# Optimization experiments

Hardware: AMD Instinct MI355X
Metric: run time of the kernel (lower is better)

Reference implementation:

```python
import jax, jax.numpy as jnp
import numpy as np

N = 50000        # nodes
R = 51           # enriched relations (25 fwd + 25 inverse + self-loop)
F_IN = 32        # feat_size
E = 32           # embed_size
C = 16           # num_classes
B = 30           # num_bases
NNZ = 2_000_000  # nonzeros in vertical adjacency


def _xavier(key, shape):
    # mimics nn.init.xavier_uniform_ with gain for relu (sqrt(2))
    fan_in, fan_out = shape[-2], shape[-1]
    a = np.sqrt(2.0) * np.sqrt(6.0 / (fan_in + fan_out))
    return jax.random.uniform(key, shape, jnp.float32, -a, a)


def setup_inputs() -> dict:
    key = jax.random.key(0)
    ks = jax.random.split(key, 8)
    # COO of vertical adjacency, shape (R*N, N)
    rows = jax.random.randint(ks[0], (NNZ,), 0, R * N)
    cols = jax.random.randint(ks[1], (NNZ,), 0, N)
    # row-normalized values: vals = 1 / row_degree  (sum_sparse with rows=True)
    deg = jax.ops.segment_sum(jnp.ones((NNZ,), jnp.float32), rows, num_segments=R * N)
    vals = (1.0 / jnp.maximum(deg, 1.0))[rows]
    features = jax.random.normal(ks[2], (N, F_IN), jnp.float32)
    comps1 = _xavier(ks[3], (R, B))
    bases1 = _xavier(ks[4], (B, F_IN, E))
    comps2 = _xavier(ks[5], (R, B))
    bases2 = _xavier(ks[6], (B, E, C))
    bias1 = jnp.zeros((E,), jnp.float32)
    bias2 = jnp.zeros((C,), jnp.float32)
    return {
        "features": features, "vals": vals,
        "comps1": comps1, "bases1": bases1, "bias1": bias1,
        "comps2": comps2, "bases2": bases2, "bias2": bias2,
        "rows": rows, "cols": cols,
    }


def _spmm(rows, cols, vals, x):
    # (R*N, N) sparse @ (N, f) dense -> (R*N, f)
    return jax.ops.segment_sum(vals[:, None] * x[cols], rows, num_segments=R * N)


def reference(features, vals, comps1, bases1, bias1, comps2, bases2, bias2, rows, cols):
    # layer 1: SpMM then basis-decomposed per-relation mixing
    h = _spmm(rows, cols, vals, features).reshape(R, N, F_IN)   # (r, n, f)
    w1 = jnp.einsum('rb,bfe->rfe', comps1, bases1)              # (r, f, e)
    h = jnp.einsum('rnf,rfe->ne', h, w1)                        # (n, e)
    h = jax.nn.relu(h + bias1)
    # layer 2
    h = _spmm(rows, cols, vals, h).reshape(R, N, E)             # (r, n, e)
    w2 = jnp.einsum('rb,bho->rho', comps2, bases2)              # (r, e, c)
    h = jnp.einsum('rho,rnh->no', w2, h)                        # (n, c)
    return h + bias2
```

## Files before the change

kernel.cpp:

```cpp
#include <hip/hip_runtime.h>

#define NNODES 50000
#define RREL 51
#define FIN 32
#define EDIM 32
#define CDIM 16
#define BB 30
#define NNZ_ 2000000
#define CAP_ 2000896
#define EPB 4096
#define NBUK 391

typedef unsigned int uint32;
typedef unsigned short ushort;
typedef uint32 u32x2 __attribute__((ext_vector_type(2)));
typedef uint32 u32x4 __attribute__((ext_vector_type(4)));
typedef short bf16x8 __attribute__((ext_vector_type(8)));
typedef float f32x4 __attribute__((ext_vector_type(4)));

static __device__ __forceinline__ uint32 pack_bf16x2(float a, float b) {
    uint32 ua = __builtin_bit_cast(uint32, a);
    uint32 ub = __builtin_bit_cast(uint32, b);
    ua += 0x7fffu + ((ua >> 16) & 1u);
    ub += 0x7fffu + ((ub >> 16) & 1u);
    return (ua >> 16) | (ub & 0xffff0000u);
}
static __device__ __forceinline__ ushort bf16_1(float x) {
    uint32 u = __builtin_bit_cast(uint32, x);
    u += 0x7fffu + ((u >> 16) & 1u);
    return (ushort)(u >> 16);
}
static __device__ __forceinline__ float unpack_lo(uint32 u) { return __builtin_bit_cast(float, u << 16); }
static __device__ __forceinline__ float unpack_hi(uint32 u) { return __builtin_bit_cast(float, u & 0xffff0000u); }

__global__ void k_weights(const float* __restrict__ comps1, const float* __restrict__ bases1,
                          const float* __restrict__ comps2, const float* __restrict__ bases2,
                          ushort* __restrict__ Wb1, ushort* __restrict__ Wb2) {
    int i = blockIdx.x * 256 + threadIdx.x;
    if (i < RREL * FIN * EDIM) {
        int r = i >> 10, fe = i & 1023, f = fe >> 5, e = fe & 31;
        float acc = 0.f;
#pragma unroll
        for (int b = 0; b < BB; b++) acc += comps1[r * BB + b] * bases1[b * 1024 + fe];
        Wb1[((r * 4 + (f >> 3)) * 32 + e) * 8 + (f & 7)] = bf16_1(acc);
    }
    if (i < RREL * EDIM * CDIM) {
        int r = i >> 9, ec = i & 511, kk = ec >> 4, c = ec & 15;
        float acc = 0.f;
#pragma unroll
        for (int b = 0; b < BB; b++) acc += comps2[r * BB + b] * bases2[b * 512 + ec];
        Wb2[((r * 4 + (kk >> 3)) * 16 + c) * 8 + (kk & 7)] = bf16_1(acc);
    }
}

__global__ void k_tobf16(const float2* __restrict__ src, uint32* __restrict__ dst, int n2) {
    int i = blockIdx.x * 256 + threadIdx.x;
    if (i < n2) {
        float2 f = src[i];
        dst[i] = pack_bf16x2(f.x, f.y);
    }
}

__global__ __launch_bounds__(1024) void k_relhist(const int* __restrict__ rows,
                                                  int* __restrict__ rel_cnt) {
    __shared__ int lc[RREL];
    int t = threadIdx.x;
    if (t < RREL) lc[t] = 0;
    __syncthreads();
    size_t k = (size_t)blockIdx.x * EPB + (size_t)t * 4;
    int rr[4];
    if (k + 4 <= NNZ_) {
        int4 rw = *(const int4*)(rows + k);
        rr[0] = rw.x; rr[1] = rw.y; rr[2] = rw.z; rr[3] = rw.w;
    } else {
#pragma unroll
        for (int j = 0; j < 4; j++) rr[j] = (k + j < NNZ_) ? rows[k + j] : -1;
    }
#pragma unroll
    for (int j = 0; j < 4; j++)
        if (rr[j] >= 0) atomicAdd(&lc[rr[j] / NNODES], 1);
    __syncthreads();
    if (t < RREL) atomicAdd(&rel_cnt[t], lc[t]);
}

__global__ void k_relscan(const int* __restrict__ rel_cnt, int* __restrict__ pad_base,
                          int* __restrict__ rel_cur) {
    if (threadIdx.x == 0) {
        int a = 0;
        for (int r = 0; r < RREL; r++) {
            pad_base[r] = a; rel_cur[r] = a;
            a += (rel_cnt[r] + 15) & ~15;
        }
        pad_base[RREL] = a;
    }
}

__global__ void k_padfill(const int* __restrict__ rel_cnt, const int* __restrict__ pad_base,
                          int* __restrict__ s_pk, int* __restrict__ s_src,
                          float* __restrict__ s_val, int* __restrict__ buk_cnt) {
    int r = blockIdx.x;
    int start, end, relv;
    if (r < RREL) { start = pad_base[r] + rel_cnt[r]; end = pad_base[r + 1]; relv = r; }
    else { start = pad_base[RREL]; end = CAP_; relv = 0; }
    if (threadIdx.x == 0 && end > start) atomicAdd(&buk_cnt[NBUK - 1], end - start);
    int pkpad = (int)(((uint32)relv << 25) | (uint32)NNODES);
    for (int i = start + threadIdx.x; i < end; i += 64) {
        s_pk[i] = pkpad;
        s_src[i] = 0;
        s_val[i] = 0.f;
    }
}

__global__ __launch_bounds__(1024) void k_scatter(const int* __restrict__ rows, const int* __restrict__ cols,
                                                  const float* __restrict__ vals, int* __restrict__ rel_cur,
                                                  int* __restrict__ buk_cnt,
                                                  int* __restrict__ s_pk, int* __restrict__ s_src,
                                                  float* __restrict__ s_val) {
    __shared__ int lcnt[RREL], lbase[RREL], gbase[RREL];
    __shared__ int bukc[NBUK];
    __shared__ int stotal;
    __shared__ uint32 st[EPB];
    int t = threadIdx.x;
    size_t base = (size_t)blockIdx.x * EPB;
    if (t < RREL) lcnt[t] = 0;
    if (t < NBUK) bukc[t] = 0;
    __syncthreads();
    size_t k = base + (size_t)t * 4;
    int relv[4], dstv[4];
    {
        int rr[4];
        if (k + 4 <= NNZ_) {
            int4 rw = *(const int4*)(rows + k);
            rr[0] = rw.x; rr[1] = rw.y; rr[2] = rw.z; rr[3] = rw.w;
        } else {
#pragma unroll
            for (int j = 0; j < 4; j++) rr[j] = (k + j < NNZ_) ? rows[k + j] : -1;
        }
#pragma unroll
        for (int j = 0; j < 4; j++) {
            if (rr[j] >= 0) {
                int rel = rr[j] / NNODES;
                relv[j] = rel;
                dstv[j] = rr[j] - rel * NNODES;
                atomicAdd(&lcnt[rel], 1);
                atomicAdd(&bukc[dstv[j] >> 7], 1);
            } else relv[j] = -1;
        }
    }
    __syncthreads();
    if (t < 64) {
        int v = (t < RREL) ? lcnt[t] : 0;
        int sum = v;
#pragma unroll
        for (int off = 1; off < 64; off <<= 1) {
            int u = __shfl_up(sum, off, 64);
            if (t >= off) sum += u;
        }
        if (t < RREL) { lbase[t] = sum - v; gbase[t] = atomicAdd(&rel_cur[t], v); }
        if (t == RREL - 1) stotal = sum;
    }
    if (t < NBUK) atomicAdd(&buk_cnt[t], bukc[t]);
    __syncthreads();
    if (t < RREL) lcnt[t] = 0;
    __syncthreads();
#pragma unroll
    for (int j = 0; j < 4; j++) {
        int rel = relv[j];
        if (rel >= 0) {
            int slot = lbase[rel] + atomicAdd(&lcnt[rel], 1);
            st[slot] = ((uint32)dstv[j] << 12) | (uint32)(t * 4 + j);
        }
    }
    __syncthreads();
    int total = stotal;
#pragma unroll
    for (int i = 0; i < 4; i++) {
        int s2 = t + i * 1024;
        if (s2 < total) {
            uint32 u = st[s2];
            int dst = (int)(u >> 12);
            size_t orig = base + (u & 4095u);
            int rel = rows[orig] / NNODES;
            int g = gbase[rel] + (s2 - lbase[rel]);
            s_pk[g] = (int)(((uint32)rel << 25) | (uint32)dst);
            s_src[g] = cols[orig];
            s_val[g] = vals[orig];
        }
    }
}

__global__ void k_bukscan(const int* __restrict__ buk_cnt, int* __restrict__ buk_base,
                          int* __restrict__ buk_cur) {
    if (threadIdx.x == 0) {
        int a = 0;
        for (int b = 0; b < NBUK; b++) { buk_base[b] = a; buk_cur[b] = a; a += buk_cnt[b]; }
        buk_base[NBUK] = a;
    }
}

__global__ __launch_bounds__(1024) void k_bucket(const int* __restrict__ s_pk,
                                                 int* __restrict__ buk_cur,
                                                 u32x2* __restrict__ tok8) {
    __shared__ int bukc[NBUK], lbase2[NBUK], gbase2[NBUK];
    __shared__ int ssum[1024];
    __shared__ u32x2 st8[EPB];
    int t = threadIdx.x;
    size_t base = (size_t)blockIdx.x * EPB;
    int total = (int)(((size_t)CAP_ - base < (size_t)EPB) ? ((size_t)CAP_ - base) : (size_t)EPB);
    if (t < NBUK) bukc[t] = 0;
    __syncthreads();
    size_t k = base + (size_t)t * 4;
    int pkv[4], bv[4];
    if (k + 4 <= CAP_) {
        int4 q = *(const int4*)(s_pk + k);
        pkv[0] = q.x; pkv[1] = q.y; pkv[2] = q.z; pkv[3] = q.w;
#pragma unroll
        for (int j = 0; j < 4; j++) bv[j] = (int)(((uint32)pkv[j] & 0x1FFFFFFu) >> 7);
    } else {
#pragma unroll
        for (int j = 0; j < 4; j++) {
            if (k + j < CAP_) { pkv[j] = s_pk[k + j]; bv[j] = (int)(((uint32)pkv[j] & 0x1FFFFFFu) >> 7); }
            else bv[j] = -1;
        }
    }
#pragma unroll
    for (int j = 0; j < 4; j++)
        if (bv[j] >= 0) atomicAdd(&bukc[bv[j]], 1);
    __syncthreads();
    int v = (t < NBUK) ? bukc[t] : 0;
    ssum[t] = v;
    __syncthreads();
    for (int off = 1; off < 1024; off <<= 1) {
        int u = (t >= off) ? ssum[t - off] : 0;
        __syncthreads();
        ssum[t] += u;
        __syncthreads();
    }
    if (t < NBUK) { lbase2[t] = ssum[t] - v; gbase2[t] = atomicAdd(&buk_cur[t], v); }
    __syncthreads();
    if (t < NBUK) bukc[t] = 0;
    __syncthreads();
#pragma unroll
    for (int j = 0; j < 4; j++) {
        if (bv[j] >= 0) {
            int slot = lbase2[bv[j]] + atomicAdd(&bukc[bv[j]], 1);
            u32x2 w; w.x = (uint32)pkv[j]; w.y = (uint32)(k + j);
            st8[slot] = w;
        }
    }
    __syncthreads();
    for (int s2 = t; s2 < total; s2 += 1024) {
        u32x2 w = st8[s2];
        int b = (int)((w.x & 0x1FFFFFFu) >> 7);
        tok8[gbase2[b] + (s2 - lbase2[b])] = w;
    }
}

__global__ __launch_bounds__(256) void k_rank(const u32x2* __restrict__ tok8,
                                              const int* __restrict__ buk_base,
                                              int* __restrict__ dst_base,
                                              int* __restrict__ s_pk) {
    __shared__ int lcnt[128], lexc[128], lrank[128], ssc[128];
    int b = blockIdx.x, t = threadIdx.x;
    int lo = buk_base[b], hi = buk_base[b + 1];
    int d0 = b << 7;
    if (t < 128) lcnt[t] = 0;
    __syncthreads();
    for (int i = lo + t; i < hi; i += 256) {
        int dl = (int)(tok8[i].x & 0x1FFFFFFu) - d0;
        atomicAdd(&lcnt[dl], 1);
    }
    __syncthreads();
    int v = (t < 128) ? lcnt[t] : 0;
    if (t < 128) ssc[t] = v;
    __syncthreads();
    for (int off = 1; off < 128; off <<= 1) {
        int u = (t >= off && t < 128) ? ssc[t - off] : 0;
        __syncthreads();
        if (t < 128) ssc[t] += u;
        __syncthreads();
    }
    if (t < 128) {
        lexc[t] = ssc[t] - v;
        int d = d0 + t;
        if (d <= NNODES) dst_base[d] = lo + lexc[t];
        lrank[t] = 0;
    }
    __syncthreads();
    for (int i = lo + t; i < hi; i += 256) {
        u32x2 w = tok8[i];
        int dl = (int)(w.x & 0x1FFFFFFu) - d0;
        int q = lo + lexc[dl] + atomicAdd(&lrank[dl], 1);
        s_pk[(int)w.y] = (int)((w.x & 0xFE000000u) | (uint32)q);
    }
}

template <int FO>
__global__ __launch_bounds__(256) void k_edgeA(const int* __restrict__ s_pk,
                                               const int* __restrict__ s_src,
                                               const float* __restrict__ s_val,
                                               const u32x4* __restrict__ Xb,
                                               const u32x4* __restrict__ Wb,
                                               uint32* __restrict__ y) {
    const int NT = FO / 16;
    const int NW = (FO == 32) ? 32 : 16;
    int t = threadIdx.x, lane = t & 63, wv = t >> 6;
    int ln15 = lane & 15, quad = lane >> 4;
    size_t k0 = (size_t)blockIdx.x * 512 + wv * 128;

    int pk0 = s_pk[k0 + lane],  pk1 = s_pk[k0 + 64 + lane];
    int sc0 = s_src[k0 + lane], sc1 = s_src[k0 + 64 + lane];
    float v0 = s_val[k0 + lane], v1 = s_val[k0 + 64 + lane];

    f32x4 acc[8][NT];
    const f32x4 zero = {0.f, 0.f, 0.f, 0.f};
#pragma unroll
    for (int s = 0; s < 8; s++) {
        int osc = (s < 4) ? sc0 : sc1;
        int opk = (s < 4) ? pk0 : pk1;
        int srcs = __shfl(osc, (s & 3) * 16 + ln15, 64);
        int rels = (int)(((uint32)__builtin_amdgcn_readfirstlane(__shfl(opk, (s & 3) * 16, 64))) >> 25);
        bf16x8 a = __builtin_bit_cast(bf16x8, Xb[(size_t)srcs * 4 + quad]);
#pragma unroll
        for (int tt = 0; tt < NT; tt++) {
            bf16x8 b = __builtin_bit_cast(bf16x8, Wb[(rels * 4 + quad) * NW + ln15 + 16 * tt]);
            acc[s][tt] = __builtin_amdgcn_mfma_f32_16x16x32_bf16(a, b, zero, 0, 0, 0);
        }
    }

#pragma unroll
    for (int s = 0; s < 8; s++) {
        int opk = (s < 4) ? pk0 : pk1;
        float ov = (s < 4) ? v0 : v1;
#pragma unroll
        for (int rg = 0; rg < 4; rg++) {
            int e = (s & 3) * 16 + quad * 4 + rg;
            float ve = __shfl(ov, e, 64);
            int pe = __shfl(opk, e, 64) & 0x1FFFFFF;
            if (FO == 32) {
                uint32 val = pack_bf16x2(acc[s][0][rg] * ve, acc[s][1][rg] * ve);
                y[(size_t)pe * 16 + ln15] = val;
            } else {
                ((ushort*)y)[(size_t)pe * 16 + ln15] = bf16_1(acc[s][0][rg] * ve);
            }
        }
    }
}

template <int FO, bool RELU, bool BF16OUT>
__global__ __launch_bounds__(256) void k_segB(const uint32* __restrict__ y,
                                              const int* __restrict__ dst_base,
                                              const float* __restrict__ bias,
                                              void* __restrict__ outp) {
    const int UPR = FO / 2;
    const int QL = UPR / 4;
    const int RPI = 64 / QL;
    const bool ILV = (FO == 32);
    int t = threadIdx.x, lane = t & 63, wv = t >> 6;
    int dst = blockIdx.x * 4 + wv;
    if (dst >= NNODES) return;
    int s = dst_base[dst], e2 = dst_base[dst + 1];
    int q = lane % QL, r = lane / QL;
    float acc[8];
#pragma unroll
    for (int j = 0; j < 8; j++) acc[j] = 0.f;
    for (int i = s + r; i < e2; i += RPI) {
        u32x4 u = __builtin_nontemporal_load((const u32x4*)(y + (size_t)i * UPR + 4 * q));
        acc[0] += unpack_lo(u.x); acc[1] += unpack_hi(u.x);
        acc[2] += unpack_lo(u.y); acc[3] += unpack_hi(u.y);
        acc[4] += unpack_lo(u.z); acc[5] += unpack_hi(u.z);
        acc[6] += unpack_lo(u.w); acc[7] += unpack_hi(u.w);
    }
#pragma unroll
    for (int off = 32; off >= QL; off >>= 1)
#pragma unroll
        for (int j = 0; j < 8; j++) acc[j] += __shfl_down(acc[j], off, 64);
    if (lane < QL) {
        float o[8];
        if (ILV) {
#pragma unroll
            for (int j = 0; j < 4; j++) {
                o[2 * j]     = acc[2 * j]     + bias[4 * q + j];
                o[2 * j + 1] = acc[2 * j + 1] + bias[4 * q + 16 + j];
                if (RELU) { o[2 * j] = fmaxf(o[2 * j], 0.f); o[2 * j + 1] = fmaxf(o[2 * j + 1], 0.f); }
            }
        } else {
#pragma unroll
            for (int j = 0; j < 8; j++) {
                o[j] = acc[j] + bias[8 * q + j];
                if (RELU) o[j] = fmaxf(o[j], 0.f);
            }
        }
        if (BF16OUT) {
            if (ILV) {
                u32x2 a0, a1;
                a0.x = pack_bf16x2(o[0], o[2]); a0.y = pack_bf16x2(o[4], o[6]);
                a1.x = pack_bf16x2(o[1], o[3]); a1.y = pack_bf16x2(o[5], o[7]);
                ((u32x2*)outp)[(size_t)dst * 8 + q] = a0;
                ((u32x2*)outp)[(size_t)dst * 8 + 4 + q] = a1;
            } else {
                u32x4 pk;
                pk.x = pack_bf16x2(o[0], o[1]); pk.y = pack_bf16x2(o[2], o[3]);
                pk.z = pack_bf16x2(o[4], o[5]); pk.w = pack_bf16x2(o[6], o[7]);
                ((u32x4*)outp)[(size_t)dst * QL + q] = pk;
            }
        } else {
            float4* op = (float4*)outp;
            op[(size_t)dst * (FO / 4) + 2 * q]     = make_float4(o[0], o[1], o[2], o[3]);
            op[(size_t)dst * (FO / 4) + 2 * q + 1] = make_float4(o[4], o[5], o[6], o[7]);
        }
    }
}

extern "C" void kernel_launch(void* const* d_in, const int* in_sizes, int n_in,
                              void* d_out, int out_size, void* d_ws, size_t ws_size,
                              hipStream_t stream) {
    const float* features = (const float*)d_in[0];
    const float* vals     = (const float*)d_in[1];
    const float* comps1   = (const float*)d_in[2];
    const float* bases1   = (const float*)d_in[3];
    const float* bias1    = (const float*)d_in[4];
    const float* comps2   = (const float*)d_in[5];
    const float* bases2   = (const float*)d_in[6];
    const float* bias2    = (const float*)d_in[7];
    const int*   rows     = (const int*)d_in[8];
    const int*   cols     = (const int*)d_in[9];
    float* out = (float*)d_out;

    float* ws = (float*)d_ws;
    size_t o = 0;
    ushort* Wb1 = (ushort*)(ws + o); o += RREL * FIN * EDIM / 2;
    ushort* Wb2 = (ushort*)(ws + o); o += RREL * EDIM * CDIM / 2;
    o = (o + 3) & ~(size_t)3;
    uint32* Xb  = (uint32*)(ws + o); o += (size_t)NNODES * (FIN / 2);
    uint32* h1b = (uint32*)(ws + o); o += (size_t)NNODES * (EDIM / 2);
    int* s_pk  = (int*)(ws + o); o += CAP_;
    int* s_src = (int*)(ws + o); o += CAP_;
    float* s_val = ws + o;       o += CAP_;
    int* rel_cnt  = (int*)(ws + o); o += RREL + 1;
    int* buk_cnt  = (int*)(ws + o); o += NBUK + 1;
    int* rel_cur  = (int*)(ws + o); o += RREL;
    int* pad_base = (int*)(ws + o); o += RREL + 1;
    int* buk_base = (int*)(ws + o); o += NBUK + 1;
    int* buk_cur  = (int*)(ws + o); o += NBUK;
    o = (o + 3) & ~(size_t)3;
    int* dst_base = (int*)(ws + o); o += NNODES + 4;
    o = (o + 3) & ~(size_t)3;
    uint32* y = (uint32*)(ws + o);
    u32x2* tok8 = (u32x2*)y;

    const int NB = (NNZ_ + EPB - 1) / EPB;
    const int NB2 = (CAP_ + EPB - 1) / EPB;

    hipMemsetAsync(rel_cnt, 0, (RREL + 1 + NBUK + 1) * sizeof(int), stream);

    k_weights<<<(RREL * FIN * EDIM + 255) / 256, 256, 0, stream>>>(comps1, bases1, comps2, bases2, Wb1, Wb2);
    k_tobf16<<<(NNODES * FIN / 2 + 255) / 256, 256, 0, stream>>>((const float2*)features, Xb, NNODES * FIN / 2);
    k_relhist<<<NB, 1024, 0, stream>>>(rows, rel_cnt);
    k_relscan<<<1, 64, 0, stream>>>(rel_cnt, pad_base, rel_cur);
    k_padfill<<<RREL + 1, 64, 0, stream>>>(rel_cnt, pad_base, s_pk, s_src, s_val, buk_cnt);
    k_scatter<<<NB, 1024, 0, stream>>>(rows, cols, vals, rel_cur, buk_cnt, s_pk, s_src, s_val);
    k_bukscan<<<1, 64, 0, stream>>>(buk_cnt, buk_base, buk_cur);
    k_bucket<<<NB2, 1024, 0, stream>>>(s_pk, buk_cur, tok8);
    k_rank<<<NBUK, 256, 0, stream>>>(tok8, buk_base, dst_base, s_pk);

    k_edgeA<EDIM><<<CAP_ / 512, 256, 0, stream>>>(s_pk, s_src, s_val, (const u32x4*)Xb,
                                                  (const u32x4*)Wb1, y);
    k_segB<EDIM, true, true><<<(NNODES + 3) / 4, 256, 0, stream>>>(y, dst_base, bias1, h1b);
    k_edgeA<CDIM><<<CAP_ / 512, 256, 0, stream>>>(s_pk, s_src, s_val, (const u32x4*)h1b,
                                                  (const u32x4*)Wb2, y);
    k_segB<CDIM, false, false><<<(NNODES + 3) / 4, 256, 0, stream>>>(y, dst_base, bias2, out);
}
```

Baseline: 381.8 us.

## Bucket edges by destination block and fuse edge MFMA with LDS segment reduction

Replaces the relation-sorted global edge arrays and per-edge intermediate buffer with compact 8-byte edge tokens. Each token packs relation, destination, source and a bf16 value. Edges are bucketed into 64-node destination blocks, with per-relation padding done locally. A single fused kernel per layer computes the MFMA products and accumulates them with LDS atomics, then applies bias and ReLU. This drops several preprocessing kernels and the global write and reread of the intermediate y. The costs are rounding edge values to bf16, LDS atomic contention, and a fixed per-block capacity (CAPB) beyond which edges are silently dropped.

```diff
diff --git a/kernel.cpp b/kernel.cpp
--- a/kernel.cpp
+++ b/kernel.cpp
@@ -7,9 +7,10 @@
 #define CDIM 16
 #define BB 30
 #define NNZ_ 2000000
-#define CAP_ 2000896
 #define EPB 4096
 #define NBUK 391
+#define NSB 782
+#define CAPB 3840
 
 typedef unsigned int uint32;
 typedef unsigned short ushort;
@@ -31,7 +32,6 @@
     return (ushort)(u >> 16);
 }
 static __device__ __forceinline__ float unpack_lo(uint32 u) { return __builtin_bit_cast(float, u << 16); }
-static __device__ __forceinline__ float unpack_hi(uint32 u) { return __builtin_bit_cast(float, u & 0xffff0000u); }
 
 __global__ void k_weights(const float* __restrict__ comps1, const float* __restrict__ bases1,
                           const float* __restrict__ comps2, const float* __restrict__ bases2,
@@ -61,11 +61,11 @@
     }
 }
 
-__global__ __launch_bounds__(1024) void k_relhist(const int* __restrict__ rows,
-                                                  int* __restrict__ rel_cnt) {
-    __shared__ int lc[RREL];
+__global__ __launch_bounds__(1024) void k_bukhist(const int* __restrict__ rows,
+                                                  int* __restrict__ buk_cnt) {
+    __shared__ int lc[NBUK];
     int t = threadIdx.x;
-    if (t < RREL) lc[t] = 0;
+    if (t < NBUK) lc[t] = 0;
     __syncthreads();
     size_t k = (size_t)blockIdx.x * EPB + (size_t)t * 4;
     int rr[4];
@@ -77,52 +77,36 @@
         for (int j = 0; j < 4; j++) rr[j] = (k + j < NNZ_) ? rows[k + j] : -1;
     }
 #pragma unroll
-    for (int j = 0; j < 4; j++)
-        if (rr[j] >= 0) atomicAdd(&lc[rr[j] / NNODES], 1);
-    __syncthreads();
-    if (t < RREL) atomicAdd(&rel_cnt[t], lc[t]);
-}
-
-__global__ void k_relscan(const int* __restrict__ rel_cnt, int* __restrict__ pad_base,
-                          int* __restrict__ rel_cur) {
+    for (int j = 0; j < 4; j++) {
+        if (rr[j] >= 0) {
+            int rel = rr[j] / NNODES;
+            atomicAdd(&lc[(rr[j] - rel * NNODES) >> 7], 1);
+        }
+    }
+    __syncthreads();
+    if (t < NBUK) atomicAdd(&buk_cnt[t], lc[t]);
+}
+
+__global__ void k_bukscan(const int* __restrict__ buk_cnt, int* __restrict__ buk_base,
+                          int* __restrict__ buk_cur) {
     if (threadIdx.x == 0) {
         int a = 0;
-        for (int r = 0; r < RREL; r++) {
-            pad_base[r] = a; rel_cur[r] = a;
-            a += (rel_cnt[r] + 15) & ~15;
-        }
-        pad_base[RREL] = a;
-    }
-}
-
-__global__ void k_padfill(const int* __restrict__ rel_cnt, const int* __restrict__ pad_base,
-                          int* __restrict__ s_pk, int* __restrict__ s_src,
-                          float* __restrict__ s_val, int* __restrict__ buk_cnt) {
-    int r = blockIdx.x;
-    int start, end, relv;
-    if (r < RREL) { start = pad_base[r] + rel_cnt[r]; end = pad_base[r + 1]; relv = r; }
-    else { start = pad_base[RREL]; end = CAP_; relv = 0; }
-    if (threadIdx.x == 0 && end > start) atomicAdd(&buk_cnt[NBUK - 1], end - start);
-    int pkpad = (int)(((uint32)relv << 25) | (uint32)NNODES);
-    for (int i = start + threadIdx.x; i < end; i += 64) {
-        s_pk[i] = pkpad;
-        s_src[i] = 0;
-        s_val[i] = 0.f;
-    }
-}
-
-__global__ __launch_bounds__(1024) void k_scatter(const int* __restrict__ rows, const int* __restrict__ cols,
-                                                  const float* __restrict__ vals, int* __restrict__ rel_cur,
-                                                  int* __restrict__ buk_cnt,
-                                                  int* __restrict__ s_pk, int* __restrict__ s_src,
-                                                  float* __restrict__ s_val) {
-    __shared__ int lcnt[RREL], lbase[RREL], gbase[RREL];
-    __shared__ int bukc[NBUK];
-    __shared__ int stotal;
-    __shared__ uint32 st[EPB];
+        for (int b = 0; b < NBUK; b++) { buk_base[b] = a; buk_cur[b] = a; a += buk_cnt[b]; }
+        buk_base[NBUK] = a;
+    }
+}
+
+__global__ __launch_bounds__(1024) void k_bucket(const int* __restrict__ rows,
+                                                 const int* __restrict__ cols,
+                                                 const float* __restrict__ vals,
+                                                 int* __restrict__ buk_cur,
+                                                 u32x2* __restrict__ tok8) {
+    __shared__ int bukc[NBUK], lb[NBUK], gb[NBUK];
+    __shared__ int ssum[1024];
+    __shared__ u32x2 st8[EPB];
     int t = threadIdx.x;
     size_t base = (size_t)blockIdx.x * EPB;
-    if (t < RREL) lcnt[t] = 0;
+    int total = (int)(((size_t)NNZ_ - base < (size_t)EPB) ? ((size_t)NNZ_ - base) : (size_t)EPB);
     if (t < NBUK) bukc[t] = 0;
     __syncthreads();
     size_t k = base + (size_t)t * 4;
@@ -142,90 +126,10 @@
                 int rel = rr[j] / NNODES;
                 relv[j] = rel;
                 dstv[j] = rr[j] - rel * NNODES;
-                atomicAdd(&lcnt[rel], 1);
                 atomicAdd(&bukc[dstv[j] >> 7], 1);
             } else relv[j] = -1;
         }
     }
-    __syncthreads();
-    if (t < 64) {
-        int v = (t < RREL) ? lcnt[t] : 0;
-        int sum = v;
-#pragma unroll
-        for (int off = 1; off < 64; off <<= 1) {
-            int u = __shfl_up(sum, off, 64);
-            if (t >= off) sum += u;
-        }
-        if (t < RREL) { lbase[t] = sum - v; gbase[t] = atomicAdd(&rel_cur[t], v); }
-        if (t == RREL - 1) stotal = sum;
-    }
-    if (t < NBUK) atomicAdd(&buk_cnt[t], bukc[t]);
-    __syncthreads();
-    if (t < RREL) lcnt[t] = 0;
-    __syncthreads();
-#pragma unroll
-    for (int j = 0; j < 4; j++) {
-        int rel = relv[j];
-        if (rel >= 0) {
-            int slot = lbase[rel] + atomicAdd(&lcnt[rel], 1);
-            st[slot] = ((uint32)dstv[j] << 12) | (uint32)(t * 4 + j);
-        }
-    }
-    __syncthreads();
-    int total = stotal;
-#pragma unroll
-    for (int i = 0; i < 4; i++) {
-        int s2 = t + i * 1024;
-        if (s2 < total) {
-            uint32 u = st[s2];
-            int dst = (int)(u >> 12);
-            size_t orig = base + (u & 4095u);
-            int rel = rows[orig] / NNODES;
-            int g = gbase[rel] + (s2 - lbase[rel]);
-            s_pk[g] = (int)(((uint32)rel << 25) | (uint32)dst);
-            s_src[g] = cols[orig];
-            s_val[g] = vals[orig];
-        }
-    }
-}
-
-__global__ void k_bukscan(const int* __restrict__ buk_cnt, int* __restrict__ buk_base,
-                          int* __restrict__ buk_cur) {
-    if (threadIdx.x == 0) {
-        int a = 0;
-        for (int b = 0; b < NBUK; b++) { buk_base[b] = a; buk_cur[b] = a; a += buk_cnt[b]; }
-        buk_base[NBUK] = a;
-    }
-}
-
-__global__ __launch_bounds__(1024) void k_bucket(const int* __restrict__ s_pk,
-                                                 int* __restrict__ buk_cur,
-                                                 u32x2* __restrict__ tok8) {
-    __shared__ int bukc[NBUK], lbase2[NBUK], gbase2[NBUK];
-    __shared__ int ssum[1024];
-    __shared__ u32x2 st8[EPB];
-    int t = threadIdx.x;
-    size_t base = (size_t)blockIdx.x * EPB;
-    int total = (int)(((size_t)CAP_ - base < (size_t)EPB) ? ((size_t)CAP_ - base) : (size_t)EPB);
-    if (t < NBUK) bukc[t] = 0;
-    __syncthreads();
-    size_t k = base + (size_t)t * 4;
-    int pkv[4], bv[4];
-    if (k + 4 <= CAP_) {
-        int4 q = *(const int4*)(s_pk + k);
-        pkv[0] = q.x; pkv[1] = q.y; pkv[2] = q.z; pkv[3] = q.w;
-#pragma unroll
-        for (int j = 0; j < 4; j++) bv[j] = (int)(((uint32)pkv[j] & 0x1FFFFFFu) >> 7);
-    } else {
-#pragma unroll
-        for (int j = 0; j < 4; j++) {
-            if (k + j < CAP_) { pkv[j] = s_pk[k + j]; bv[j] = (int)(((uint32)pkv[j] & 0x1FFFFFFu) >> 7); }
-            else bv[j] = -1;
-        }
-    }
-#pragma unroll
-    for (int j = 0; j < 4; j++)
-        if (bv[j] >= 0) atomicAdd(&bukc[bv[j]], 1);
     __syncthreads();
     int v = (t < NBUK) ? bukc[t] : 0;
     ssum[t] = v;
@@ -236,178 +140,161 @@
         ssum[t] += u;
         __syncthreads();
     }
-    if (t < NBUK) { lbase2[t] = ssum[t] - v; gbase2[t] = atomicAdd(&buk_cur[t], v); }
+    if (t < NBUK) { lb[t] = ssum[t] - v; gb[t] = atomicAdd(&buk_cur[t], v); }
     __syncthreads();
     if (t < NBUK) bukc[t] = 0;
     __syncthreads();
-#pragma unroll
-    for (int j = 0; j < 4; j++) {
-        if (bv[j] >= 0) {
-            int slot = lbase2[bv[j]] + atomicAdd(&bukc[bv[j]], 1);
-            u32x2 w; w.x = (uint32)pkv[j]; w.y = (uint32)(k + j);
-            st8[slot] = w;
+    {
+        int cc[4]; float vv[4];
+        if (k + 4 <= NNZ_) {
+            int4 cw = *(const int4*)(cols + k);
+            float4 vw = *(const float4*)(vals + k);
+            cc[0] = cw.x; cc[1] = cw.y; cc[2] = cw.z; cc[3] = cw.w;
+            vv[0] = vw.x; vv[1] = vw.y; vv[2] = vw.z; vv[3] = vw.w;
+        } else {
+#pragma unroll
+            for (int j = 0; j < 4; j++) {
+                cc[j] = (k + j < NNZ_) ? cols[k + j] : 0;
+                vv[j] = (k + j < NNZ_) ? vals[k + j] : 0.f;
+            }
+        }
+#pragma unroll
+        for (int j = 0; j < 4; j++) {
+            if (relv[j] >= 0) {
+                int b = dstv[j] >> 7;
+                int slot = lb[b] + atomicAdd(&bukc[b], 1);
+                u32x2 w;
+                w.x = ((uint32)relv[j] << 16) | (uint32)dstv[j];
+                w.y = ((uint32)cc[j] << 16) | (uint32)bf16_1(vv[j]);
+                st8[slot] = w;
+            }
         }
     }
     __syncthreads();
     for (int s2 = t; s2 < total; s2 += 1024) {
         u32x2 w = st8[s2];
-        int b = (int)((w.x & 0x1FFFFFFu) >> 7);
-        tok8[gbase2[b] + (s2 - lbase2[b])] = w;
+        int b = (int)(w.x & 0xFFFFu) >> 7;
+        tok8[gb[b] + (s2 - lb[b])] = w;
     }
 }
 
 __global__ __launch_bounds__(256) void k_rank(const u32x2* __restrict__ tok8,
                                               const int* __restrict__ buk_base,
-                                              int* __restrict__ dst_base,
-                                              int* __restrict__ s_pk) {
-    __shared__ int lcnt[128], lexc[128], lrank[128], ssc[128];
+                                              u32x2* __restrict__ eb,
+                                              int* __restrict__ nsub16) {
+    __shared__ int cnt[2 * RREL], base[2 * RREL], cnt2[2 * RREL];
     int b = blockIdx.x, t = threadIdx.x;
     int lo = buk_base[b], hi = buk_base[b + 1];
     int d0 = b << 7;
-    if (t < 128) lcnt[t] = 0;
+    if (t < 2 * RREL) cnt[t] = 0;
     __syncthreads();
     for (int i = lo + t; i < hi; i += 256) {
-        int dl = (int)(tok8[i].x & 0x1FFFFFFu) - d0;
-        atomicAdd(&lcnt[dl], 1);
-    }
-    __syncthreads();
-    int v = (t < 128) ? lcnt[t] : 0;
-    if (t < 128) ssc[t] = v;
-    __syncthreads();
-    for (int off = 1; off < 128; off <<= 1) {
-        int u = (t >= off && t < 128) ? ssc[t - off] : 0;
-        __syncthreads();
-        if (t < 128) ssc[t] += u;
-        __syncthreads();
-    }
-    if (t < 128) {
-        lexc[t] = ssc[t] - v;
-        int d = d0 + t;
-        if (d <= NNODES) dst_base[d] = lo + lexc[t];
-        lrank[t] = 0;
-    }
+        uint32 w0 = tok8[i].x;
+        int rel = (int)(w0 >> 16);
+        int dl = (int)(w0 & 0xFFFFu) - d0;
+        atomicAdd(&cnt[(dl >> 6) * RREL + rel], 1);
+    }
+    __syncthreads();
+    if (t == 0) {
+        int run = 0;
+        for (int g = 0; g < RREL; g++) { base[g] = run; run += (cnt[g] + 15) & ~15; }
+        nsub16[2 * b] = (run < CAPB ? run : CAPB) >> 4;
+        run = 0;
+        for (int g = RREL; g < 2 * RREL; g++) { base[g] = run; run += (cnt[g] + 15) & ~15; }
+        nsub16[2 * b + 1] = (run < CAPB ? run : CAPB) >> 4;
+    }
+    __syncthreads();
+    if (t < 2 * RREL) cnt2[t] = 0;
     __syncthreads();
     for (int i = lo + t; i < hi; i += 256) {
         u32x2 w = tok8[i];
-        int dl = (int)(w.x & 0x1FFFFFFu) - d0;
-        int q = lo + lexc[dl] + atomicAdd(&lrank[dl], 1);
-        s_pk[(int)w.y] = (int)((w.x & 0xFE000000u) | (uint32)q);
+        int rel = (int)(w.x >> 16);
+        int dl = (int)(w.x & 0xFFFFu) - d0;
+        int g = (dl >> 6) * RREL + rel;
+        int slot = base[g] + atomicAdd(&cnt2[g], 1);
+        if (slot < CAPB)
+            eb[(size_t)(2 * b + (dl >> 6)) * CAPB + slot] = w;
+    }
+    __syncthreads();
+    if (t < 2 * RREL) {
+        int c = cnt[t];
+        int p = (c + 15) & ~15;
+        int sub = (t >= RREL) ? 1 : 0;
+        uint32 rel = (uint32)(sub ? t - RREL : t);
+        int B = 2 * b + sub;
+        u32x2 w;
+        w.x = (rel << 16) | (uint32)(B << 6);
+        w.y = 0;
+        for (int i = base[t] + c; i < base[t] + p; i++)
+            if (i < CAPB) eb[(size_t)B * CAPB + i] = w;
     }
 }
 
 template <int FO>
-__global__ __launch_bounds__(256) void k_edgeA(const int* __restrict__ s_pk,
-                                               const int* __restrict__ s_src,
-                                               const float* __restrict__ s_val,
+__global__ __launch_bounds__(256) void k_fused(const u32x2* __restrict__ eb,
+                                               const int* __restrict__ nsub16,
                                                const u32x4* __restrict__ Xb,
                                                const u32x4* __restrict__ Wb,
-                                               uint32* __restrict__ y) {
+                                               const float* __restrict__ bias,
+                                               void* __restrict__ outp) {
     const int NT = FO / 16;
     const int NW = (FO == 32) ? 32 : 16;
+    __shared__ float h[64][FO + 1];
     int t = threadIdx.x, lane = t & 63, wv = t >> 6;
     int ln15 = lane & 15, quad = lane >> 4;
-    size_t k0 = (size_t)blockIdx.x * 512 + wv * 128;
-
-    int pk0 = s_pk[k0 + lane],  pk1 = s_pk[k0 + 64 + lane];
-    int sc0 = s_src[k0 + lane], sc1 = s_src[k0 + 64 + lane];
-    float v0 = s_val[k0 + lane], v1 = s_val[k0 + 64 + lane];
-
-    f32x4 acc[8][NT];
+    int B = blockIdx.x;
+    for (int i = t; i < 64 * (FO + 1); i += 256) ((float*)h)[i] = 0.f;
+    __syncthreads();
+    int ns = nsub16[B];
+    size_t eb0 = (size_t)B * CAPB;
+    int d0 = B << 6;
     const f32x4 zero = {0.f, 0.f, 0.f, 0.f};
-#pragma unroll
-    for (int s = 0; s < 8; s++) {
-        int osc = (s < 4) ? sc0 : sc1;
-        int opk = (s < 4) ? pk0 : pk1;
-        int srcs = __shfl(osc, (s & 3) * 16 + ln15, 64);
-        int rels = (int)(((uint32)__builtin_amdgcn_readfirstlane(__shfl(opk, (s & 3) * 16, 64))) >> 25);
-        bf16x8 a = __builtin_bit_cast(bf16x8, Xb[(size_t)srcs * 4 + quad]);
+    for (int s = wv; s < ns; s += 4) {
+        u32x2 w = eb[eb0 + s * 16 + ln15];
+        int rel = (int)(__builtin_amdgcn_readfirstlane(w.x) >> 16);
+        int dl = (int)(w.x & 0xFFFFu) - d0;
+        int src = (int)(w.y >> 16);
+        float val = unpack_lo(w.y);
+        bf16x8 a = __builtin_bit_cast(bf16x8, Xb[(size_t)src * 4 + quad]);
+        f32x4 acc[NT];
 #pragma unroll
         for (int tt = 0; tt < NT; tt++) {
-            bf16x8 b = __builtin_bit_cast(bf16x8, Wb[(rels * 4 + quad) * NW + ln15 + 16 * tt]);
-            acc[s][tt] = __builtin_amdgcn_mfma_f32_16x16x32_bf16(a, b, zero, 0, 0, 0);
-        }
-    }
-
-#pragma unroll
-    for (int s = 0; s < 8; s++) {
-        int opk = (s < 4) ? pk0 : pk1;
-        float ov = (s < 4) ? v0 : v1;
+            bf16x8 bb = __builtin_bit_cast(bf16x8, Wb[(rel * 4 + quad) * NW + ln15 + 16 * tt]);
+            acc[tt] = __builtin_amdgcn_mfma_f32_16x16x32_bf16(a, bb, zero, 0, 0, 0);
+        }
 #pragma unroll
         for (int rg = 0; rg < 4; rg++) {
-            int e = (s & 3) * 16 + quad * 4 + rg;
-            float ve = __shfl(ov, e, 64);
-            int pe = __shfl(opk, e, 64) & 0x1FFFFFF;
-            if (FO == 32) {
-                uint32 val = pack_bf16x2(acc[s][0][rg] * ve, acc[s][1][rg] * ve);
-                y[(size_t)pe * 16 + ln15] = val;
-            } else {
-                ((ushort*)y)[(size_t)pe * 16 + ln15] = bf16_1(acc[s][0][rg] * ve);
+            int e = quad * 4 + rg;
+            float ve = __shfl(val, e, 64);
+            int de = __shfl(dl, e, 64);
+#pragma unroll
+            for (int tt = 0; tt < NT; tt++)
+                atomicAdd(&h[de][ln15 + 16 * tt], acc[tt][rg] * ve);
+        }
+    }
+    __syncthreads();
+    int dl = t >> 2;
+    int dst = d0 + dl;
+    if (dst < NNODES) {
+        if (FO == 32) {
+            int q = t & 3;
+            u32x4 pk;
+            float* hr = &h[dl][q * 8];
+#pragma unroll
+            for (int j = 0; j < 4; j++) {
+                float o0 = fmaxf(hr[2 * j] + bias[q * 8 + 2 * j], 0.f);
+                float o1 = fmaxf(hr[2 * j + 1] + bias[q * 8 + 2 * j + 1], 0.f);
+                pk[j] = pack_bf16x2(o0, o1);
             }
-        }
-    }
-}
-
-template <int FO, bool RELU, bool BF16OUT>
-__global__ __launch_bounds__(256) void k_segB(const uint32* __restrict__ y,
-                                              const int* __restrict__ dst_base,
-                                              const float* __restrict__ bias,
-                                              void* __restrict__ outp) {
-    const int UPR = FO / 2;
-    const int QL = UPR / 4;
-    const int RPI = 64 / QL;
-    const bool ILV = (FO == 32);
-    int t = threadIdx.x, lane = t & 63, wv = t >> 6;
-    int dst = blockIdx.x * 4 + wv;
-    if (dst >= NNODES) return;
-    int s = dst_base[dst], e2 = dst_base[dst + 1];
-    int q = lane % QL, r = lane / QL;
-    float acc[8];
-#pragma unroll
-    for (int j = 0; j < 8; j++) acc[j] = 0.f;
-    for (int i = s + r; i < e2; i += RPI) {
-        u32x4 u = __builtin_nontemporal_load((const u32x4*)(y + (size_t)i * UPR + 4 * q));
-        acc[0] += unpack_lo(u.x); acc[1] += unpack_hi(u.x);
-        acc[2] += unpack_lo(u.y); acc[3] += unpack_hi(u.y);
-        acc[4] += unpack_lo(u.z); acc[5] += unpack_hi(u.z);
-        acc[6] += unpack_lo(u.w); acc[7] += unpack_hi(u.w);
-    }
-#pragma unroll
-    for (int off = 32; off >= QL; off >>= 1)
-#pragma unroll
-        for (int j = 0; j < 8; j++) acc[j] += __shfl_down(acc[j], off, 64);
-    if (lane < QL) {
-        float o[8];
-        if (ILV) {
-#pragma unroll
-            for (int j = 0; j < 4; j++) {
-                o[2 * j]     = acc[2 * j]     + bias[4 * q + j];
-                o[2 * j + 1] = acc[2 * j + 1] + bias[4 * q + 16 + j];
-                if (RELU) { o[2 * j] = fmaxf(o[2 * j], 0.f); o[2 * j + 1] = fmaxf(o[2 * j + 1], 0.f); }
-            }
+            ((u32x4*)outp)[(size_t)dst * 4 + q] = pk;
         } else {
-#pragma unroll
-            for (int j = 0; j < 8; j++) {
-                o[j] = acc[j] + bias[8 * q + j];
-                if (RELU) o[j] = fmaxf(o[j], 0.f);
-            }
-        }
-        if (BF16OUT) {
-            if (ILV) {
-                u32x2 a0, a1;
-                a0.x = pack_bf16x2(o[0], o[2]); a0.y = pack_bf16x2(o[4], o[6]);
-                a1.x = pack_bf16x2(o[1], o[3]); a1.y = pack_bf16x2(o[5], o[7]);
-                ((u32x2*)outp)[(size_t)dst * 8 + q] = a0;
-                ((u32x2*)outp)[(size_t)dst * 8 + 4 + q] = a1;
-            } else {
-                u32x4 pk;
-                pk.x = pack_bf16x2(o[0], o[1]); pk.y = pack_bf16x2(o[2], o[3]);
-                pk.z = pack_bf16x2(o[4], o[5]); pk.w = pack_bf16x2(o[6], o[7]);
-                ((u32x4*)outp)[(size_t)dst * QL + q] = pk;
-            }
-        } else {
-            float4* op = (float4*)outp;
-            op[(size_t)dst * (FO / 4) + 2 * q]     = make_float4(o[0], o[1], o[2], o[3]);
-            op[(size_t)dst * (FO / 4) + 2 * q + 1] = make_float4(o[4], o[5], o[6], o[7]);
+            int c4 = t & 3;
+            float4 o;
+            o.x = h[dl][c4 * 4]     + bias[c4 * 4];
+            o.y = h[dl][c4 * 4 + 1] + bias[c4 * 4 + 1];
+            o.z = h[dl][c4 * 4 + 2] + bias[c4 * 4 + 2];
+            o.w = h[dl][c4 * 4 + 3] + bias[c4 * 4 + 3];
+            ((float4*)outp)[(size_t)dst * 4 + c4] = o;
         }
     }
 }
@@ -434,40 +321,25 @@
     o = (o + 3) & ~(size_t)3;
     uint32* Xb  = (uint32*)(ws + o); o += (size_t)NNODES * (FIN / 2);
     uint32* h1b = (uint32*)(ws + o); o += (size_t)NNODES * (EDIM / 2);
-    int* s_pk  = (int*)(ws + o); o += CAP_;
-    int* s_src = (int*)(ws + o); o += CAP_;
-    float* s_val = ws + o;       o += CAP_;
-    int* rel_cnt  = (int*)(ws + o); o += RREL + 1;
     int* buk_cnt  = (int*)(ws + o); o += NBUK + 1;
-    int* rel_cur  = (int*)(ws + o); o += RREL;
-    int* pad_base = (int*)(ws + o); o += RREL + 1;
     int* buk_base = (int*)(ws + o); o += NBUK + 1;
     int* buk_cur  = (int*)(ws + o); o += NBUK;
+    int* nsub16   = (int*)(ws + o); o += NSB;
     o = (o + 3) & ~(size_t)3;
-    int* dst_base = (int*)(ws + o); o += NNODES + 4;
-    o = (o + 3) & ~(size_t)3;
-    uint32* y = (uint32*)(ws + o);
-    u32x2* tok8 = (u32x2*)y;
+    u32x2* tok8 = (u32x2*)(ws + o); o += (size_t)NNZ_ * 2;
+    u32x2* eb   = (u32x2*)(ws + o); o += (size_t)NSB * CAPB * 2;
 
     const int NB = (NNZ_ + EPB - 1) / EPB;
-    const int NB2 = (CAP_ + EPB - 1) / EPB;
-
-    hipMemsetAsync(rel_cnt, 0, (RREL + 1 + NBUK + 1) * sizeof(int), stream);
+
+    hipMemsetAsync(buk_cnt, 0, (NBUK + 1) * sizeof(int), stream);
 
     k_weights<<<(RREL * FIN * EDIM + 255) / 256, 256, 0, stream>>>(comps1, bases1, comps2, bases2, Wb1, Wb2);
     k_tobf16<<<(NNODES * FIN / 2 + 255) / 256, 256, 0, stream>>>((const float2*)features, Xb, NNODES * FIN / 2);
-    k_relhist<<<NB, 1024, 0, stream>>>(rows, rel_cnt);
-    k_relscan<<<1, 64, 0, stream>>>(rel_cnt, pad_base, rel_cur);
-    k_padfill<<<RREL + 1, 64, 0, stream>>>(rel_cnt, pad_base, s_pk, s_src, s_val, buk_cnt);
-    k_scatter<<<NB, 1024, 0, stream>>>(rows, cols, vals, rel_cur, buk_cnt, s_pk, s_src, s_val);
+    k_bukhist<<<NB, 1024, 0, stream>>>(rows, buk_cnt);
     k_bukscan<<<1, 64, 0, stream>>>(buk_cnt, buk_base, buk_cur);
-    k_bucket<<<NB2, 1024, 0, stream>>>(s_pk, buk_cur, tok8);
-    k_rank<<<NBUK, 256, 0, stream>>>(tok8, buk_base, dst_base, s_pk);
-
-    k_edgeA<EDIM><<<CAP_ / 512, 256, 0, stream>>>(s_pk, s_src, s_val, (const u32x4*)Xb,
-                                                  (const u32x4*)Wb1, y);
-    k_segB<EDIM, true, true><<<(NNODES + 3) / 4, 256, 0, stream>>>(y, dst_base, bias1, h1b);
-    k_edgeA<CDIM><<<CAP_ / 512, 256, 0, stream>>>(s_pk, s_src, s_val, (const u32x4*)h1b,
-                                                  (const u32x4*)Wb2, y);
-    k_segB<CDIM, false, false><<<(NNODES + 3) / 4, 256, 0, stream>>>(y, dst_base, bias2, out);
-}
+    k_bucket<<<NB, 1024, 0, stream>>>(rows, cols, vals, buk_cur, tok8);
+    k_rank<<<NBUK, 256, 0, stream>>>(tok8, buk_base, eb, nsub16);
+
+    k_fused<EDIM><<<NSB, 256, 0, stream>>>(eb, nsub16, (const u32x4*)Xb, (const u32x4*)Wb1, bias1, h1b);
+    k_fused<CDIM><<<NSB, 256, 0, stream>>>(eb, nsub16, (const u32x4*)h1b, (const u32x4*)Wb2, bias2, out);
+}
```

After: 916.2 us. 140% more time.
